# Kernel tuning notes

Hardware: AMD Instinct MI355X
Metric: run time of the kernel (lower is better)

Reference implementation:

```python
import jax, jax.numpy as jnp
import numpy as np

T, B, IN_DIM = 1024, 8, 512
D_VALUE, D_KEY = 64, 64
V_TH = 1.0
EPS = 1e-08


def setup_inputs() -> dict:
    key = jax.random.key(0)
    ks = jax.random.split(key, 7)
    s_in = 1.0 / np.sqrt(IN_DIM)
    x = jax.random.normal(ks[0], (T, B, IN_DIM), dtype=jnp.float32)
    Wv = jax.random.uniform(ks[1], (D_VALUE, IN_DIM), jnp.float32, -s_in, s_in)
    bv = jax.random.uniform(ks[2], (D_VALUE,), jnp.float32, -s_in, s_in)
    Wk = jax.random.uniform(ks[3], (D_KEY, IN_DIM), jnp.float32, -s_in, s_in)
    bk = jax.random.uniform(ks[4], (D_KEY,), jnp.float32, -s_in, s_in)
    Wa = jax.random.uniform(ks[5], (D_KEY, IN_DIM), jnp.float32, -s_in, s_in)
    ba = jax.random.uniform(ks[6], (D_KEY,), jnp.float32, -s_in, s_in)
    return {"x": x, "Wv": Wv, "bv": bv, "Wk": Wk, "bk": bk, "Wa": Wa, "ba": ba}


def reference(x, Wv, bv, Wk, bk, Wa, ba):
    # projections: v (T,B,d), k (T,B,n), alpha (T,B,n)
    v = jnp.einsum('tbi,di->tbd', x, Wv) + bv
    k = jnp.einsum('tbi,ni->tbn', x, Wk) + bk
    alpha = jax.nn.sigmoid(jnp.einsum('tbi,ni->tbn', x, Wa) + ba)
    # outer-product writes: (T,B,d,n)
    writes = jnp.einsum('tbd,tbn->tbdn', v, k)
    # closed-form linear recurrence S_t = S_{t-1} * alpha_t + writes_t via cumprod/cumsum
    P = jnp.cumprod(alpha, axis=0)                       # (T,B,n)
    invP = 1.0 / (P + EPS)
    scaled = writes * invP[:, :, None, :]                # (T,B,d,n)
    S = jnp.cumsum(scaled, axis=0) * P[:, :, None, :]    # (T,B,d,n)
    Tt, Bb = x.shape[0], x.shape[1]
    mem = S.reshape(Tt, Bb, D_VALUE * D_KEY)
    spk = (mem > V_TH).astype(mem.dtype)
    return spk, mem
```

## Files before the change

### kernel.cpp

```cpp
#include <hip/hip_runtime.h>
#include <cmath>

#define TT 1024
#define BB 8
#define IND 512
#define NCH 32
#define CHL 32
#define EPSV 1e-8
#define OUTHALF ((size_t)TT * BB * 4096)

__global__ __launch_bounds__(256)
void k1_proj(const float* __restrict__ x,
             const float* __restrict__ Wv, const float* __restrict__ bv,
             const float* __restrict__ Wk, const float* __restrict__ bk,
             const float* __restrict__ Wa, const float* __restrict__ ba,
             float* __restrict__ vOut, float* __restrict__ kOut,
             float* __restrict__ aOut)
{
    __shared__ float sWt[64][192];
    __shared__ float sXt[64][16];
    const int tid = threadIdx.x;
    const int rowbase = blockIdx.x * 16;
    const int c0 = tid & 63;
    const int r0 = (tid >> 6) << 2;
    double a0[4] = {}, a1[4] = {}, a2[4] = {};

    for (int ko = 0; ko < IND; ko += 64) {
        __syncthreads();
        if (tid < 192) {
            const float* src = (tid < 64  ? Wv + (size_t)tid * IND
                              : tid < 128 ? Wk + (size_t)(tid - 64) * IND
                              :             Wa + (size_t)(tid - 128) * IND) + ko;
            #pragma unroll
            for (int q = 0; q < 64; q += 4) {
                float4 w4 = *(const float4*)(src + q);
                sWt[q+0][tid] = w4.x; sWt[q+1][tid] = w4.y;
                sWt[q+2][tid] = w4.z; sWt[q+3][tid] = w4.w;
            }
        }
        {
            int r  = tid & 15;
            int kq = (tid >> 4) << 2;
            float4 x4 = *(const float4*)(x + (size_t)(rowbase + r) * IND + ko + kq);
            sXt[kq+0][r] = x4.x; sXt[kq+1][r] = x4.y;
            sXt[kq+2][r] = x4.z; sXt[kq+3][r] = x4.w;
        }
        __syncthreads();

        float f0[4] = {}, f1[4] = {}, f2[4] = {};
        #pragma unroll
        for (int q = 0; q < 64; ++q) {
            float4 xv = *(const float4*)&sXt[q][r0];
            float w0 = sWt[q][c0], w1 = sWt[q][c0 + 64], w2 = sWt[q][c0 + 128];
            f0[0] = fmaf(xv.x, w0, f0[0]); f1[0] = fmaf(xv.x, w1, f1[0]); f2[0] = fmaf(xv.x, w2, f2[0]);
            f0[1] = fmaf(xv.y, w0, f0[1]); f1[1] = fmaf(xv.y, w1, f1[1]); f2[1] = fmaf(xv.y, w2, f2[1]);
            f0[2] = fmaf(xv.z, w0, f0[2]); f1[2] = fmaf(xv.z, w1, f1[2]); f2[2] = fmaf(xv.z, w2, f2[2]);
            f0[3] = fmaf(xv.w, w0, f0[3]); f1[3] = fmaf(xv.w, w1, f1[3]); f2[3] = fmaf(xv.w, w2, f2[3]);
        }
        #pragma unroll
        for (int i = 0; i < 4; ++i) { a0[i] += f0[i]; a1[i] += f1[i]; a2[i] += f2[i]; }
    }

    #pragma unroll
    for (int i = 0; i < 4; ++i) {
        int r = rowbase + r0 + i;
        vOut[r * 64 + c0] = (float)(a0[i] + (double)bv[c0]);
        kOut[r * 64 + c0] = (float)(a1[i] + (double)bk[c0]);
        double z = a2[i] + (double)ba[c0];
        aOut[r * 64 + c0] = (float)(1.0 / (1.0 + exp(-z)));
    }
}

__global__ __launch_bounds__(64)
void kPF(const float* __restrict__ alpha, double* __restrict__ cpA)
{
    int chain = blockIdx.x * 64 + threadIdx.x;
    double run = 1.0;
    for (int ch = 0; ch < NCH; ++ch) {
        cpA[ch * 512 + chain] = run;
        double p = 1.0;
        #pragma unroll
        for (int t = 0; t < CHL; ++t)
            p *= (double)alpha[(ch * CHL + t) * 512 + chain];
        run *= p;
    }
}

__global__ __launch_bounds__(256)
void k3_csum(const float* __restrict__ vIn, const float* __restrict__ kIn,
             const float* __restrict__ alpha, const double* __restrict__ cpA,
             double* __restrict__ Csum)
{
    __shared__ double sV[CHL * 64];
    const int tid = threadIdx.x;
    const int ch = blockIdx.x >> 3;
    const int b  = blockIdx.x & 7;
    #pragma unroll
    for (int q = 0; q < 8; ++q) {
        int idx = q * 256 + tid;
        int ti = idx >> 6, d = idx & 63;
        sV[idx] = (double)vIn[(((ch * CHL + ti) * BB) + b) * 64 + d];
    }
    __syncthreads();
    const int n = tid & 63;
    const int w = tid >> 6;
    double P = cpA[ch * 512 + b * 64 + n];
    double C[16];
    #pragma unroll
    for (int j = 0; j < 16; ++j) C[j] = 0.0;
    for (int i = 0; i < CHL; ++i) {
        int base = ((ch * CHL + i) * BB + b) * 64 + n;
        P *= (double)alpha[base];
        double invp = 1.0 / (P + EPSV);
        double kd = (double)kIn[base] * invp;
        const double* vrow = &sV[i * 64 + w * 16];
        #pragma unroll
        for (int j = 0; j < 16; ++j) C[j] = fma(vrow[j], kd, C[j]);
    }
    size_t cb = ((size_t)ch * 8 + b) * 4096 + (size_t)w * 1024 + n;
    #pragma unroll
    for (int j = 0; j < 16; ++j) Csum[cb + j * 64] = C[j];
}

__global__ __launch_bounds__(256)
void k3b_prefix(double* __restrict__ Csum)
{
    int s = blockIdx.x * 256 + threadIdx.x;
    int b = s >> 12, rest = s & 4095;
    double run = 0.0;
    for (int ch = 0; ch < NCH; ++ch) {
        size_t idx = ((size_t)ch * 8 + b) * 4096 + rest;
        double t = Csum[idx];
        Csum[idx] = run;
        run += t;
    }
}

__global__ __launch_bounds__(256)
void k4_scan(const float* __restrict__ vIn, const float* __restrict__ kIn,
             const float* __restrict__ alpha, const double* __restrict__ cpA,
             const double* __restrict__ Csum, float* __restrict__ outp)
{
    __shared__ double sV[CHL * 64];
    const int tid = threadIdx.x;
    const int ch = blockIdx.x >> 3;
    const int b  = blockIdx.x & 7;
    #pragma unroll
    for (int q = 0; q < 8; ++q) {
        int idx = q * 256 + tid;
        int ti = idx >> 6, d = idx & 63;
        sV[idx] = (double)vIn[(((ch * CHL + ti) * BB) + b) * 64 + d];
    }
    __syncthreads();
    const int n = tid & 63;
    const int w = tid >> 6;
    double P = cpA[ch * 512 + b * 64 + n];
    size_t cb = ((size_t)ch * 8 + b) * 4096 + (size_t)w * 1024 + n;
    double C[16];
    #pragma unroll
    for (int j = 0; j < 16; ++j) C[j] = Csum[cb + j * 64];

    float* spk = outp;
    float* mem = outp + OUTHALF;
    for (int i = 0; i < CHL; ++i) {
        int t = ch * CHL + i;
        int base = (t * BB + b) * 64 + n;
        P *= (double)alpha[base];
        double invp = 1.0 / (P + EPSV);
        double kd = (double)kIn[base] * invp;
        const double* vrow = &sV[i * 64 + w * 16];
        size_t ob = ((size_t)t * BB + b) * 4096 + (size_t)w * 1024 + n;
        #pragma unroll
        for (int j = 0; j < 16; ++j) {
            C[j] = fma(vrow[j], kd, C[j]);
            double S = P * C[j];
            mem[ob + j * 64] = (float)S;
            spk[ob + j * 64] = (S > 1.0) ? 1.0f : 0.0f;
        }
    }
}

extern "C" void kernel_launch(void* const* d_in, const int* in_sizes, int n_in,
                              void* d_out, int out_size, void* d_ws, size_t ws_size,
                              hipStream_t stream)
{
    const float* x  = (const float*)d_in[0];
    const float* Wv = (const float*)d_in[1];
    const float* bv = (const float*)d_in[2];
    const float* Wk = (const float*)d_in[3];
    const float* bk = (const float*)d_in[4];
    const float* Wa = (const float*)d_in[5];
    const float* ba = (const float*)d_in[6];
    float* out = (float*)d_out;

    char* ws = (char*)d_ws;
    float*  v     = (float*)(ws);
    float*  kk    = (float*)(ws + (2u << 20));
    float*  alpha = (float*)(ws + (4u << 20));
    double* cpA   = (double*)(ws + (6u << 20));
    double* Csum  = (double*)(ws + (7u << 20));

    hipLaunchKernelGGL(k1_proj,    dim3(512), dim3(256), 0, stream,
                       x, Wv, bv, Wk, bk, Wa, ba, v, kk, alpha);
    hipLaunchKernelGGL(kPF,        dim3(8),   dim3(64),  0, stream, alpha, cpA);
    hipLaunchKernelGGL(k3_csum,    dim3(256), dim3(256), 0, stream,
                       v, kk, alpha, cpA, Csum);
    hipLaunchKernelGGL(k3b_prefix, dim3(128), dim3(256), 0, stream, Csum);
    hipLaunchKernelGGL(k4_scan,    dim3(256), dim3(256), 0, stream,
                       v, kk, alpha, cpA, Csum, out);
}
```

Measured before the change: 130.4 us.

## Fold serial chunk-prefix product kernel into scan kernels via redundant recomputation

Removes the kPF kernel, which computed chunk-start cumulative alpha products using only 8 blocks of 64 threads walking 1024 timesteps serially. Each block of k3_csum and k4_scan now recomputes its starting product directly from alpha using four independent product accumulators. The load is issued before the barrier so it overlaps the shared-memory fill. The prefix kernel is also changed to load all chunk values up front to expose memory-level parallelism. The trade-off is redundant global reads of alpha (up to 1024 per thread in late chunks), and products are now multiplied in a different order, which slightly changes the rounding.

```diff
diff --git a/kernel.cpp b/kernel.cpp
--- a/kernel.cpp
+++ b/kernel.cpp
@@ -71,25 +71,23 @@
     }
 }
 
-__global__ __launch_bounds__(64)
-void kPF(const float* __restrict__ alpha, double* __restrict__ cpA)
-{
-    int chain = blockIdx.x * 64 + threadIdx.x;
-    double run = 1.0;
-    for (int ch = 0; ch < NCH; ++ch) {
-        cpA[ch * 512 + chain] = run;
-        double p = 1.0;
-        #pragma unroll
-        for (int t = 0; t < CHL; ++t)
-            p *= (double)alpha[(ch * CHL + t) * 512 + chain];
-        run *= p;
-    }
+__device__ __forceinline__ double flatP(const float* __restrict__ alpha,
+                                        int b, int n, int tmax)
+{
+    const float* ap = alpha + b * 64 + n;
+    double p0 = 1.0, p1 = 1.0, p2 = 1.0, p3 = 1.0;
+    for (int t = 0; t < tmax; t += 4) {
+        p0 *= (double)ap[(size_t)(t + 0) * 512];
+        p1 *= (double)ap[(size_t)(t + 1) * 512];
+        p2 *= (double)ap[(size_t)(t + 2) * 512];
+        p3 *= (double)ap[(size_t)(t + 3) * 512];
+    }
+    return (p0 * p1) * (p2 * p3);
 }
 
 __global__ __launch_bounds__(256)
 void k3_csum(const float* __restrict__ vIn, const float* __restrict__ kIn,
-             const float* __restrict__ alpha, const double* __restrict__ cpA,
-             double* __restrict__ Csum)
+             const float* __restrict__ alpha, double* __restrict__ Csum)
 {
     __shared__ double sV[CHL * 64];
     const int tid = threadIdx.x;
@@ -101,10 +99,10 @@
         int ti = idx >> 6, d = idx & 63;
         sV[idx] = (double)vIn[(((ch * CHL + ti) * BB) + b) * 64 + d];
     }
-    __syncthreads();
     const int n = tid & 63;
     const int w = tid >> 6;
-    double P = cpA[ch * 512 + b * 64 + n];
+    double P = flatP(alpha, b, n, ch * CHL);
+    __syncthreads();
     double C[16];
     #pragma unroll
     for (int j = 0; j < 16; ++j) C[j] = 0.0;
@@ -127,19 +125,22 @@
 {
     int s = blockIdx.x * 256 + threadIdx.x;
     int b = s >> 12, rest = s & 4095;
+    double vals[NCH];
+    #pragma unroll
+    for (int ch = 0; ch < NCH; ++ch)
+        vals[ch] = Csum[((size_t)ch * 8 + b) * 4096 + rest];
     double run = 0.0;
+    #pragma unroll
     for (int ch = 0; ch < NCH; ++ch) {
-        size_t idx = ((size_t)ch * 8 + b) * 4096 + rest;
-        double t = Csum[idx];
-        Csum[idx] = run;
-        run += t;
+        Csum[((size_t)ch * 8 + b) * 4096 + rest] = run;
+        run += vals[ch];
     }
 }
 
 __global__ __launch_bounds__(256)
 void k4_scan(const float* __restrict__ vIn, const float* __restrict__ kIn,
-             const float* __restrict__ alpha, const double* __restrict__ cpA,
-             const double* __restrict__ Csum, float* __restrict__ outp)
+             const float* __restrict__ alpha, const double* __restrict__ Csum,
+             float* __restrict__ outp)
 {
     __shared__ double sV[CHL * 64];
     const int tid = threadIdx.x;
@@ -151,10 +152,10 @@
         int ti = idx >> 6, d = idx & 63;
         sV[idx] = (double)vIn[(((ch * CHL + ti) * BB) + b) * 64 + d];
     }
-    __syncthreads();
     const int n = tid & 63;
     const int w = tid >> 6;
-    double P = cpA[ch * 512 + b * 64 + n];
+    double P = flatP(alpha, b, n, ch * CHL);
+    __syncthreads();
     size_t cb = ((size_t)ch * 8 + b) * 4096 + (size_t)w * 1024 + n;
     double C[16];
     #pragma unroll
@@ -197,15 +198,13 @@
     float*  v     = (float*)(ws);
     float*  kk    = (float*)(ws + (2u << 20));
     float*  alpha = (float*)(ws + (4u << 20));
-    double* cpA   = (double*)(ws + (6u << 20));
-    double* Csum  = (double*)(ws + (7u << 20));
+    double* Csum  = (double*)(ws + (6u << 20));
 
     hipLaunchKernelGGL(k1_proj,    dim3(512), dim3(256), 0, stream,
                        x, Wv, bv, Wk, bk, Wa, ba, v, kk, alpha);
-    hipLaunchKernelGGL(kPF,        dim3(8),   dim3(64),  0, stream, alpha, cpA);
     hipLaunchKernelGGL(k3_csum,    dim3(256), dim3(256), 0, stream,
-                       v, kk, alpha, cpA, Csum);
+                       v, kk, alpha, Csum);
     hipLaunchKernelGGL(k3b_prefix, dim3(128), dim3(256), 0, stream, Csum);
     hipLaunchKernelGGL(k4_scan,    dim3(256), dim3(256), 0, stream,
-                       v, kk, alpha, cpA, Csum, out);
-}
+                       v, kk, alpha, Csum, out);
+}
```

After: 218.9 us. 67.9% more time.
